# Optimization experiments

Hardware: AMD Instinct MI355X
Metric: run time of the kernel (lower is better)

## Reference

```python
import jax, jax.numpy as jnp
import numpy as np

WALL, SRC_REAL, SRC_IMAG, DELAY_REAL, DELAY_IMAG = 0, 1, 2, 3, 4
DELAY_STEP = 8
MAX_PHASE_NORM = 2.0
READOUT_THRESHOLD = 0.35
PHASE_CLASSES = 8


def conv2d(x, w, b, pad):
    y = jax.lax.conv_general_dilated(x, w, (1, 1), [(pad, pad), (pad, pad)],
                                     dimension_numbers=('NCHW', 'OIHW', 'NCHW'))
    return y + b[None, :, None, None]


def clamp_phase(r, i):
    mag = jnp.sqrt(r * r + i * i + 1e-8)
    s = jnp.minimum(MAX_PHASE_NORM / mag, 1.0)
    return r * s, i * s


def neighbor_sum(x):
    # zero-padded 4-neighbor shift-and-sum stencil
    p = jnp.pad(x, ((0, 0), (0, 0), (1, 1), (1, 1)))
    return (p[:, :, 2:, 1:-1] + p[:, :, :-2, 1:-1] +
            p[:, :, 1:-1, 2:] + p[:, :, 1:-1, :-2])


def setup_inputs() -> dict:
    key = jax.random.key(0)
    ks = jax.random.split(key, 8)
    B, H, W, WD = 8, 256, 256, 32
    CIN = 6 + 4  # INPUT_CHANNELS + 4 (state_r, state_i, frontier_r, frontier_i)
    x = jax.random.normal(ks[0], (B, 6, H, W), jnp.float32)
    target = jax.random.randint(ks[1], (B, 2), 0, H)
    w_in = jax.random.normal(ks[2], (WD, CIN, 1, 1), jnp.float32) * (1.0 / np.sqrt(CIN))
    b_in = jnp.zeros((WD,), jnp.float32)
    w_up = jax.random.normal(ks[3], (WD, WD + CIN, 3, 3), jnp.float32) * (1.0 / np.sqrt((WD + CIN) * 9))
    b_up = jnp.zeros((WD,), jnp.float32)
    w_gate = jax.random.normal(ks[4], (1, WD + CIN, 1, 1), jnp.float32) * (1.0 / np.sqrt(WD + CIN))
    b_gate = jnp.zeros((1,), jnp.float32)
    angle = jnp.float32(0.0)
    decay_logit = jnp.float32(3.9)
    return dict(x=x, target=target, w_in=w_in, b_in=b_in, w_up=w_up, b_up=b_up,
                w_gate=w_gate, b_gate=b_gate, angle=angle, decay_logit=decay_logit, steps=16)


def reference(x, target, w_in, b_in, w_up, b_up, w_gate, b_gate, angle, decay_logit, steps):
    wall = x[:, WALL:WALL + 1]
    free = 1.0 - wall
    state_r = x[:, SRC_REAL:SRC_REAL + 1] * free
    state_i = x[:, SRC_IMAG:SRC_IMAG + 1] * free
    frontier_r, frontier_i = state_r, state_i
    h = jnp.tanh(conv2d(jnp.concatenate([x, state_r, state_i, frontier_r, frontier_i], 1), w_in, b_in, 0)) * free

    ang = jnp.tanh(angle) * 0.02
    cos_a, sin_a = jnp.cos(ang), jnp.sin(ang)
    decay = 0.95 + 0.05 * jax.nn.sigmoid(decay_logit)
    delay_r = x[:, DELAY_REAL:DELAY_REAL + 1]
    delay_i = x[:, DELAY_IMAG:DELAY_IMAG + 1]

    def body(carry, step):
        s_r, s_i, f_r, f_i, hh = carry
        inc_r = neighbor_sum(f_r)
        inc_i = neighbor_sum(f_i)
        is_delay = (step == DELAY_STEP).astype(x.dtype)
        inc_r = inc_r + is_delay * delay_r
        inc_i = inc_i + is_delay * delay_i
        source = jnp.concatenate([hh, x, s_r, s_i, f_r, f_i], 1)
        g = 0.998 + 0.002 * jax.nn.sigmoid(conv2d(source, w_gate, b_gate, 0))
        inc_r = inc_r * g
        inc_i = inc_i * g
        rot_r = inc_r * cos_a - inc_i * sin_a
        rot_i = inc_r * sin_a + inc_i * cos_a
        inc_r, inc_i = rot_r * free, rot_i * free
        inc_r, inc_i = clamp_phase(inc_r, inc_i)
        pre_wall = ((jnp.abs(inc_r) + jnp.abs(inc_i)) * wall).mean()
        s_r, s_i = clamp_phase(decay * s_r + inc_r, decay * s_i + inc_i)
        s_r = s_r * free
        s_i = s_i * free
        hh = jnp.tanh(0.8 * hh + conv2d(source, w_up, b_up, 1)) * free
        st = jnp.concatenate([s_r, s_i], 1)
        return (s_r, s_i, inc_r, inc_i, hh), (st, pre_wall)

    carry0 = (state_r, state_i, frontier_r, frontier_i, h)
    _, (sts, pre_walls) = jax.lax.scan(body, carry0, jnp.arange(1, steps + 1))
    state0 = jnp.concatenate([state_r, state_i], 1)
    states = jnp.concatenate([state0[None], sts], 0)  # [steps+1, B, 2, H, W]
    final = states[-1]

    diffs = states[1:] - states[:-1]
    delta = jnp.mean(jnp.sqrt(jnp.mean(diffs ** 2, axis=(1, 2, 3, 4))))
    norm_by_step = jnp.mean(jnp.sqrt(jnp.sum(states ** 2, axis=2)))
    sat = (jnp.abs(final) > 4.0).astype(jnp.float32).mean()
    pw = pre_walls.mean()
    norm = jnp.sqrt(jnp.sum(final ** 2, axis=1, keepdims=True))
    leak = ((norm > 0.5) & (wall > 0.5)).astype(jnp.float32).mean()
    stats = jnp.stack([delta, norm_by_step, sat, pw, leak])

    b = jnp.arange(final.shape[0])
    vec = final[b, :, target[:, 0], target[:, 1]]  # [B, 2]
    k = jnp.arange(PHASE_CLASSES)
    theta = 2.0 * jnp.pi * k / PHASE_CLASSES
    phases = jnp.stack([jnp.cos(theta), jnp.sin(theta)], axis=1)  # [K, 2]
    mag = jnp.sqrt(jnp.sum(vec ** 2, axis=1) + 1e-8)
    none = (READOUT_THRESHOLD - mag) * 12.0
    phase_logits = (vec @ phases.T - READOUT_THRESHOLD) * 12.0
    logits = jnp.concatenate([none[:, None], phase_logits], axis=1)
    return logits, stats
```

## Files before the change

### kernel.cpp

```cpp
#include <hip/hip_runtime.h>
#include <hip/hip_bf16.h>

#define HW2D 65536
#define NPIX 524288
#define NB 8
#define PW 258
#define PP 66564
#define NSTEPS 16
#define RHH 2064
#define RTT 4128
#define ROWB 8256

typedef __hip_bfloat16 bf16;
typedef unsigned long long u64;
typedef __attribute__((ext_vector_type(8))) short short8;
typedef __attribute__((ext_vector_type(4))) float f32x4;

__device__ __forceinline__ unsigned short f2bfu(float v){
  bf16 h = __float2bfloat16(v); return *(unsigned short*)&h;
}
__device__ __forceinline__ float blo(unsigned int w){ return __uint_as_float(w<<16); }
__device__ __forceinline__ float bhi(unsigned int w){ return __uint_as_float(w & 0xffff0000u); }
__device__ __forceinline__ float tanh_a(float z){
  return z*__builtin_amdgcn_rsqf(fmaf(z, z, 1.0f));
}
__device__ __forceinline__ float fast_sigmoid(float z){
  return 1.0f/(1.0f + __expf(-z));
}
__device__ __forceinline__ unsigned char f2fp8(float v){
  return (unsigned char)(__builtin_amdgcn_cvt_pk_fp8_f32(v, 0.f, 0, false) & 0xFF);
}
__device__ __forceinline__ int chmap(int m){ return (m>>1) + (m&1)*16; }

__global__ void k_setup(const float* __restrict__ w_up, const float* __restrict__ w_gate,
                        const float* angle, const float* decay_logit,
                        u64* __restrict__ WB8, short8* __restrict__ WB16,
                        float* ST, float* PRM){
  int t = threadIdx.x;
  for (int i = t; i < 64*32; i += 256) ST[i] = 0.0f;
  if (t == 0){
    float ang = tanhf(angle[0])*0.02f;
    PRM[0] = cosf(ang);
    PRM[1] = sinf(ang);
    PRM[2] = 0.95f + 0.05f/(1.0f+expf(-decay_logit[0]));
  }
  int lane = t & 63;
  int r_ = lane & 15, g = lane >> 4;
  for (int slot = t>>6; slot < 19; slot += 4){
    u64 v = 0;
    #pragma unroll
    for (int j=0;j<8;j++){
      float w = 0.f;
      int ch = chmap(g*8+j);
      if (slot < 18){
        int tile = slot/9, s = slot%9;
        int oc = tile*16 + r_;
        int dy=s/3, dx=s%3;
        w = w_up[((oc*42+ch)*3+dy)*3+dx];
        if (s==4 && oc==ch) w += 0.8f;
      } else {
        if (r_==0) w = w_gate[ch];
      }
      v |= ((u64)f2fp8(w)) << (8*j);
    }
    WB8[slot*64+lane] = v;
  }
  for (int slot = t>>6; slot < 11; slot += 4){
    short8 v;
    #pragma unroll
    for (int j=0;j<8;j++){
      float w = 0.f;
      int tt = (g&1)*8 + j;
      int tapsel = g>>1;
      if (slot < 10){
        int tile = slot/5, s2 = slot%5;
        int tap = 2*s2 + tapsel;
        int oc = tile*16 + r_;
        if (tap <= 8 && tt < 10){
          int src = (tt<4) ? (38+tt) : (32+(tt-4));
          int dy=tap/3, dx=tap%3;
          w = w_up[((oc*42+src)*3+dy)*3+dx];
        }
      } else {
        if (r_==0 && tapsel==0 && tt<10){
          int src = (tt<4) ? (38+tt) : (32+(tt-4));
          w = w_gate[src];
        }
      }
      v[j] = (short)f2bfu(w);
    }
    WB16[slot*64+lane] = v;
  }
}

__global__ void k_init(const float* __restrict__ x, const float* __restrict__ w_in,
                       const float* __restrict__ b_in,
                       float* __restrict__ WALL,
                       unsigned char* __restrict__ HH0, unsigned char* __restrict__ HH1,
                       unsigned char* __restrict__ TAIL0, unsigned char* __restrict__ TAIL1,
                       float* ST){
  int tid = threadIdx.x;
  int i = blockIdx.x*256 + tid;
  float v = 0.0f;
  if (i < NB*PP){
    int b = i / PP, pp_ = i % PP;
    int row = pp_ / PW, col = pp_ % PW;
    size_t rb = (size_t)(b*PW + row);
    if (row == 0 || row == 257 || col == 0 || col == 257){
      #pragma unroll
      for (int g=0; g<4; g++){
        size_t a = (rb*4+g)*RHH + (size_t)col*8;
        *(uint2*)(HH0+a) = (uint2){0,0};
        *(uint2*)(HH1+a) = (uint2){0,0};
      }
      #pragma unroll
      for (int h=0; h<2; h++){
        size_t a = (rb*2+h)*RTT + (size_t)col*16;
        *(uint4*)(TAIL0+a) = (uint4){0,0,0,0};
        *(uint4*)(TAIL1+a) = (uint4){0,0,0,0};
      }
    } else {
      int y = row-1, xc = col-1;
      int rem = (y<<8) + xc;
      const float* xb = x + (size_t)b*6*HW2D;
      float wall = xb[rem];
      float fre = 1.0f - wall;
      float s_r = xb[HW2D + rem]*fre;
      float s_i = xb[2*HW2D + rem]*fre;
      WALL[b*HW2D + rem] = wall;
      float src10[10];
      src10[0]=wall;
      #pragma unroll
      for (int c=1;c<6;c++) src10[c]=xb[c*HW2D+rem];
      src10[6]=s_r; src10[7]=s_i; src10[8]=s_r; src10[9]=s_i;
      float hv[32];
      #pragma unroll
      for (int c=0;c<32;c++){
        float a = b_in[c];
        #pragma unroll
        for (int k=0;k<10;k++) a += w_in[c*10+k]*src10[k];
        hv[c] = tanh_a(a)*fre;
      }
      unsigned int words[8];
      #pragma unroll
      for (int w=0;w<8;w++){
        int lo = __builtin_amdgcn_cvt_pk_fp8_f32(hv[2*w], hv[16+2*w], 0, false);
        words[w] = (unsigned int)__builtin_amdgcn_cvt_pk_fp8_f32(hv[2*w+1], hv[17+2*w], lo, true);
      }
      #pragma unroll
      for (int g=0; g<4; g++){
        *(uint2*)(HH0 + (rb*4+g)*RHH + (size_t)col*8) = (uint2){words[2*g], words[2*g+1]};
      }
      unsigned short tv[16];
      tv[0]=f2bfu(s_r); tv[1]=f2bfu(s_i); tv[2]=f2bfu(s_r); tv[3]=f2bfu(s_i);
      #pragma unroll
      for (int c=0;c<6;c++) tv[4+c] = f2bfu(src10[c]);
      #pragma unroll
      for (int c=10;c<16;c++) tv[c] = 0;
      #pragma unroll
      for (int h=0; h<2; h++){
        short8 vv;
        #pragma unroll
        for (int j=0;j<8;j++) vv[j] = (short)tv[h*8+j];
        *(short8*)(TAIL0 + (rb*2+h)*RTT + (size_t)col*16) = vv;
        *(short8*)(TAIL1 + (rb*2+h)*RTT + (size_t)col*16) = vv;
      }
      v = __builtin_amdgcn_sqrtf(s_r*s_r + s_i*s_i);
    }
  }
  #pragma unroll
  for (int off=32; off>0; off>>=1) v += __shfl_down(v, off);
  if ((tid&63)==0 && v != 0.0f)
    atomicAdd(&ST[(blockIdx.x & 63)*32 + 16], v);
}

__global__ __launch_bounds__(256) void k_step(
    const unsigned char* __restrict__ HHo, unsigned char* __restrict__ HHn,
    const unsigned char* __restrict__ TAILo, unsigned char* __restrict__ TAILn,
    const float* __restrict__ WALL,
    const u64* __restrict__ WB8, const short8* __restrict__ WB16,
    const float* __restrict__ b_up, const float* __restrict__ x,
    const float* __restrict__ b_gate, const float* __restrict__ PRM,
    float* ST, int step){
  int bid = blockIdx.x;
  int b = bid & 7, y = bid >> 3;
  int tid = threadIdx.x;
  int wv = tid >> 6, lane = tid & 63;
  int r_ = lane & 15, g = lane >> 4;
  int px0 = wv*64 + r_;

  const unsigned char* Tc = TAILo + (size_t)(b*PW + y + 1)*ROWB + (size_t)(tid+1)*16;
  unsigned int sw  = *(const unsigned int*)(Tc);
  unsigned int fu  = *(const unsigned int*)(Tc - ROWB + 4);
  unsigned int fd  = *(const unsigned int*)(Tc + ROWB + 4);
  unsigned int fl  = *(const unsigned int*)(Tc - 16 + 4);
  unsigned int fr2 = *(const unsigned int*)(Tc + 16 + 4);
  float dlr = 0.f, dli = 0.f;
  if (step==8){
    const float* xb = x + (size_t)b*6*HW2D;
    int rem = (y<<8)+tid;
    dlr = xb[3*HW2D+rem]; dli = xb[4*HW2D+rem];
  }
  float wallB = WALL[b*HW2D + (y<<8) + tid];
  float ca = PRM[0], sa = PRM[1], dec = PRM[2];

  const unsigned char* Hrow = HHo + (size_t)(b*PW + y)*ROWB + (size_t)g*RHH + (size_t)px0*8;
  const unsigned char* Trow = TAILo + (size_t)(b*PW + y)*ROWB + (size_t)(g&1)*RTT + (size_t)px0*16;
  const unsigned char* Tzero = TAILo + (size_t)(b*PW)*ROWB + (size_t)(g&1)*RTT + (size_t)px0*16;
  int gb = g >> 1;
  const unsigned char* tb0 = Trow + (size_t)((0+gb)/3)*ROWB + (size_t)((0+gb)%3)*16;
  const unsigned char* tb1 = Trow + (size_t)((2+gb)/3)*ROWB + (size_t)((2+gb)%3)*16;
  const unsigned char* tb2 = Trow + (size_t)((4+gb)/3)*ROWB + (size_t)((4+gb)%3)*16;
  const unsigned char* tb3 = Trow + (size_t)((6+gb)/3)*ROWB + (size_t)((6+gb)%3)*16;
  const unsigned char* tb4 = gb ? Tzero : (Trow + 2*ROWB + 2*16);
  const u64* wb8l = WB8 + lane;
  const short8* wb16l = WB16 + lane;

  f32x4 acc[4][2], accg[4];
  #pragma unroll
  for (int mt=0;mt<4;mt++){
    acc[mt][0] = (f32x4){0.f,0.f,0.f,0.f};
    acc[mt][1] = (f32x4){0.f,0.f,0.f,0.f};
    accg[mt]   = (f32x4){0.f,0.f,0.f,0.f};
  }

  __builtin_amdgcn_s_setprio(1);
  #pragma unroll
  for (int s=0;s<9;s++){
    u64 b0 = wb8l[s*64], b1 = wb8l[(9+s)*64];
    u64 aH[4];
    #pragma unroll
    for (int mt=0;mt<4;mt++)
      aH[mt] = *(const u64*)(Hrow + (size_t)((s/3)*ROWB) + ((s%3)*8 + mt*128));
    #pragma unroll
    for (int mt=0;mt<4;mt++){
      acc[mt][0] = __builtin_amdgcn_mfma_f32_16x16x32_fp8_fp8((long)b0, (long)aH[mt], acc[mt][0], 0,0,0);
      acc[mt][1] = __builtin_amdgcn_mfma_f32_16x16x32_fp8_fp8((long)b1, (long)aH[mt], acc[mt][1], 0,0,0);
    }
    if (s==4){
      u64 bg = wb8l[18*64];
      #pragma unroll
      for (int mt=0;mt<4;mt++)
        accg[mt] = __builtin_amdgcn_mfma_f32_16x16x32_fp8_fp8((long)bg, (long)aH[mt], accg[mt], 0,0,0);
    }
  }
  #pragma unroll
  for (int s2=0;s2<5;s2++){
    short8 b0 = wb16l[s2*64], b1 = wb16l[(5+s2)*64];
    const unsigned char* tb = (s2==0)?tb0:(s2==1)?tb1:(s2==2)?tb2:(s2==3)?tb3:tb4;
    short8 aT[4];
    #pragma unroll
    for (int mt=0;mt<4;mt++)
      aT[mt] = *(const short8*)(tb + mt*256);
    #pragma unroll
    for (int mt=0;mt<4;mt++){
      acc[mt][0] = __builtin_amdgcn_mfma_f32_16x16x32_bf16(b0, aT[mt], acc[mt][0], 0,0,0);
      acc[mt][1] = __builtin_amdgcn_mfma_f32_16x16x32_bf16(b1, aT[mt], acc[mt][1], 0,0,0);
    }
    if (s2==2){
      short8 bgt = wb16l[10*64];
      #pragma unroll
      for (int mt=0;mt<4;mt++)
        accg[mt] = __builtin_amdgcn_mfma_f32_16x16x32_bf16(bgt, aT[mt], accg[mt], 0,0,0);
    }
  }
  __builtin_amdgcn_s_setprio(0);

  float ga0 = __shfl(accg[0][0], r_);
  float ga1 = __shfl(accg[1][0], r_);
  float ga2 = __shfl(accg[2][0], r_);
  float ga3 = __shfl(accg[3][0], r_);
  float gpre = (g==0) ? ga0 : (g==1) ? ga1 : (g==2) ? ga2 : ga3;

  const float* wallrow = WALL + (size_t)b*HW2D + (y<<8);
  const float4* bup4 = (const float4*)b_up;
  float4 bb0 = bup4[g];
  float4 bb1 = bup4[4+g];
  unsigned char* Hn = HHn + ((size_t)(b*PW + y + 1)*4 + g)*RHH;
  #pragma unroll
  for (int mt=0;mt<4;mt++){
    int px = px0 + mt*16;
    float fre = 1.0f - wallrow[px];
    float tA0 = tanh_a(acc[mt][0][0] + bb0.x)*fre;
    float tB0 = tanh_a(acc[mt][1][0] + bb1.x)*fre;
    float tA1 = tanh_a(acc[mt][0][1] + bb0.y)*fre;
    float tB1 = tanh_a(acc[mt][1][1] + bb1.y)*fre;
    float tA2 = tanh_a(acc[mt][0][2] + bb0.z)*fre;
    float tB2 = tanh_a(acc[mt][1][2] + bb1.z)*fre;
    float tA3 = tanh_a(acc[mt][0][3] + bb0.w)*fre;
    float tB3 = tanh_a(acc[mt][1][3] + bb1.w)*fre;
    int w0 = __builtin_amdgcn_cvt_pk_fp8_f32(tA0, tB0, 0, false);
    w0 = __builtin_amdgcn_cvt_pk_fp8_f32(tA1, tB1, w0, true);
    int w1 = __builtin_amdgcn_cvt_pk_fp8_f32(tA2, tB2, 0, false);
    w1 = __builtin_amdgcn_cvt_pk_fp8_f32(tA3, tB3, w1, true);
    *(uint2*)(Hn + (size_t)(px+1)*8) = (uint2){(unsigned)w0, (unsigned)w1};
  }

  float s_r = blo(sw), s_i = bhi(sw);
  float incr = blo(fu) + blo(fd) + blo(fl) + blo(fr2) + dlr;
  float inci = bhi(fu) + bhi(fd) + bhi(fl) + bhi(fr2) + dli;
  float fre = 1.0f - wallB;
  float a = gpre + b_gate[0];
  float gg = 0.998f + 0.002f*fast_sigmoid(a);
  incr *= gg; inci *= gg;
  float rr = incr*ca - inci*sa;
  float ri = incr*sa + inci*ca;
  incr = rr*fre; inci = ri*fre;
  float m1 = fmaf(incr,incr, fmaf(inci,inci, 1e-8f));
  float sc2 = fminf(2.0f*__builtin_amdgcn_rsqf(m1), 1.0f);
  incr *= sc2; inci *= sc2;
  float pw = (fabsf(incr)+fabsf(inci))*wallB;
  float nr = dec*s_r + incr, ni = dec*s_i + inci;
  float m2 = fmaf(nr,nr, fmaf(ni,ni, 1e-8f));
  sc2 = fminf(2.0f*__builtin_amdgcn_rsqf(m2), 1.0f);
  nr = nr*sc2*fre; ni = ni*sc2*fre;
  ushort4 pk;
  pk.x = f2bfu(nr); pk.y = f2bfu(ni); pk.z = f2bfu(incr); pk.w = f2bfu(inci);
  *(ushort4*)(TAILn + (size_t)(b*PW + y + 1)*ROWB + (size_t)(tid+1)*16) = pk;
  float d2 = (nr-s_r)*(nr-s_r)+(ni-s_i)*(ni-s_i);
  float nrm = __builtin_amdgcn_sqrtf(nr*nr+ni*ni);
  #pragma unroll
  for (int off=32; off>0; off>>=1){
    d2  += __shfl_down(d2, off);
    nrm += __shfl_down(nrm, off);
    pw  += __shfl_down(pw, off);
  }
  if (step==16){
    float sat = (fabsf(nr)>4.0f ? 1.0f:0.0f) + (fabsf(ni)>4.0f ? 1.0f:0.0f);
    float nn = __builtin_amdgcn_sqrtf(nr*nr+ni*ni);
    float leak = (nn>0.5f && wallB>0.5f) ? 1.0f : 0.0f;
    #pragma unroll
    for (int off=32; off>0; off>>=1){
      sat  += __shfl_down(sat, off);
      leak += __shfl_down(leak, off);
    }
    if (lane==0){
      float* st = ST + ((bid*4+wv) & 63)*32;
      atomicAdd(&st[18], sat);
      atomicAdd(&st[19], leak);
    }
  }
  if (lane==0){
    float* st = ST + ((bid*4+wv) & 63)*32;
    atomicAdd(&st[step-1], d2);
    atomicAdd(&st[16],     nrm);
    atomicAdd(&st[17],     pw);
  }
}

__global__ void k_final(const unsigned char* __restrict__ TAIL, const int* __restrict__ target,
                        const float* __restrict__ ST, float* __restrict__ out){
  int t = threadIdx.x;
  if (t < 8){
    int ty = target[2*t], tx = target[2*t+1];
    unsigned int sw = *(const unsigned int*)(TAIL + (size_t)(t*PW+ty+1)*ROWB + (size_t)(tx+1)*16);
    float vr = blo(sw), vi = bhi(sw);
    float mag = sqrtf(vr*vr+vi*vi+1e-8f);
    out[t*9] = (0.35f - mag)*12.0f;
    #pragma unroll
    for (int k=0;k<8;k++){
      float th = 6.283185307179586f * (float)k / 8.0f;
      out[t*9+1+k] = (vr*cosf(th)+vi*sinf(th) - 0.35f)*12.0f;
    }
  }
  float tot[20];
  #pragma unroll
  for (int i=0;i<20;i++){
    float v = ST[t*32 + i];
    #pragma unroll
    for (int off=32; off>0; off>>=1) v += __shfl_down(v, off);
    tot[i] = v;
  }
  if (t == 0){
    float d = 0.0f;
    #pragma unroll
    for (int s=0;s<16;s++) d += sqrtf(tot[s]/1048576.0f);
    out[72] = d/16.0f;
    out[73] = tot[16]/8912896.0f;
    out[74] = tot[18]/1048576.0f;
    out[75] = tot[17]/(524288.0f*16.0f);
    out[76] = tot[19]/524288.0f;
  }
}

extern "C" void kernel_launch(void* const* d_in, const int* in_sizes, int n_in,
                              void* d_out, int out_size, void* d_ws, size_t ws_size,
                              hipStream_t stream) {
  const float* x       = (const float*)d_in[0];
  const int*   target  = (const int*)  d_in[1];
  const float* w_in    = (const float*)d_in[2];
  const float* b_in    = (const float*)d_in[3];
  const float* w_up    = (const float*)d_in[4];
  const float* b_up    = (const float*)d_in[5];
  const float* w_gate  = (const float*)d_in[6];
  const float* b_gate  = (const float*)d_in[7];
  const float* angle   = (const float*)d_in[8];
  const float* decay_l = (const float*)d_in[9];
  float* out = (float*)d_out;

  char* ws = (char*)d_ws;
  size_t off = 0;
  unsigned char* HH0 = (unsigned char*)(ws+off); off += (size_t)NB*PP*32;
  unsigned char* HH1 = (unsigned char*)(ws+off); off += (size_t)NB*PP*32;
  unsigned char* TAIL0=(unsigned char*)(ws+off); off += (size_t)NB*PP*32;
  unsigned char* TAIL1=(unsigned char*)(ws+off); off += (size_t)NB*PP*32;
  float* WALL = (float*)(ws+off); off += (size_t)NPIX*4;
  u64* WB8 = (u64*)(ws+off); off += (size_t)19*64*8;
  short8* WB16 = (short8*)(ws+off); off += (size_t)11*64*16;
  float* ST = (float*)(ws+off); off += (size_t)64*32*4;
  float* PRM = (float*)(ws+off); off += 16*4;

  k_setup<<<1,256,0,stream>>>(w_up, w_gate, angle, decay_l, WB8, WB16, ST, PRM);
  k_init<<<(NB*PP+255)/256,256,0,stream>>>(x, w_in, b_in, WALL, HH0, HH1,
                                           TAIL0, TAIL1, ST);

  unsigned char *hho=HH0, *hhn=HH1, *tlo=TAIL0, *tln=TAIL1;
  for (int t=1;t<=NSTEPS;t++){
    k_step<<<2048,256,0,stream>>>(hho, hhn, tlo, tln, WALL,
                                  WB8, WB16, b_up, x, b_gate, PRM, ST, t);
    unsigned char* tc=hho; hho=hhn; hhn=tc;
    tc=tlo; tlo=tln; tln=tc;
  }
  k_final<<<1,64,0,stream>>>(tlo, target, ST, out);
}
```

Baseline: 504.3 us.

## Split step kernel across 8 waves, passing gate through shared memory

Doubles the block size of the step kernel to 512 threads so each wave computes 32 pixels (2 MFMA tiles) instead of 64. This cuts per-thread accumulator registers and raises the number of waves available to hide memory latency. Because wave and pixel indices no longer line up, the gate pre-activation is passed through LDS behind a block barrier, and only the first 256 threads run the stencil and state update. In exchange it adds a barrier, leaves half the threads idle in the elementwise tail, and loads weights redundantly in more waves.

Result: slower. 580.5 us (+15.1%).

```diff
diff --git a/kernel.cpp b/kernel.cpp
--- a/kernel.cpp
+++ b/kernel.cpp
@@ -174,7 +174,7 @@
     atomicAdd(&ST[(blockIdx.x & 63)*32 + 16], v);
 }
 
-__global__ __launch_bounds__(256) void k_step(
+__global__ __launch_bounds__(512) void k_step(
     const unsigned char* __restrict__ HHo, unsigned char* __restrict__ HHn,
     const unsigned char* __restrict__ TAILo, unsigned char* __restrict__ TAILn,
     const float* __restrict__ WALL,
@@ -182,27 +182,13 @@
     const float* __restrict__ b_up, const float* __restrict__ x,
     const float* __restrict__ b_gate, const float* __restrict__ PRM,
     float* ST, int step){
+  __shared__ float lgate[256];
   int bid = blockIdx.x;
   int b = bid & 7, y = bid >> 3;
   int tid = threadIdx.x;
   int wv = tid >> 6, lane = tid & 63;
   int r_ = lane & 15, g = lane >> 4;
-  int px0 = wv*64 + r_;
-
-  const unsigned char* Tc = TAILo + (size_t)(b*PW + y + 1)*ROWB + (size_t)(tid+1)*16;
-  unsigned int sw  = *(const unsigned int*)(Tc);
-  unsigned int fu  = *(const unsigned int*)(Tc - ROWB + 4);
-  unsigned int fd  = *(const unsigned int*)(Tc + ROWB + 4);
-  unsigned int fl  = *(const unsigned int*)(Tc - 16 + 4);
-  unsigned int fr2 = *(const unsigned int*)(Tc + 16 + 4);
-  float dlr = 0.f, dli = 0.f;
-  if (step==8){
-    const float* xb = x + (size_t)b*6*HW2D;
-    int rem = (y<<8)+tid;
-    dlr = xb[3*HW2D+rem]; dli = xb[4*HW2D+rem];
-  }
-  float wallB = WALL[b*HW2D + (y<<8) + tid];
-  float ca = PRM[0], sa = PRM[1], dec = PRM[2];
+  int px0 = wv*32 + r_;
 
   const unsigned char* Hrow = HHo + (size_t)(b*PW + y)*ROWB + (size_t)g*RHH + (size_t)px0*8;
   const unsigned char* Trow = TAILo + (size_t)(b*PW + y)*ROWB + (size_t)(g&1)*RTT + (size_t)px0*16;
@@ -216,135 +202,152 @@
   const u64* wb8l = WB8 + lane;
   const short8* wb16l = WB16 + lane;
 
-  f32x4 acc[4][2], accg[4];
-  #pragma unroll
-  for (int mt=0;mt<4;mt++){
-    acc[mt][0] = (f32x4){0.f,0.f,0.f,0.f};
-    acc[mt][1] = (f32x4){0.f,0.f,0.f,0.f};
-    accg[mt]   = (f32x4){0.f,0.f,0.f,0.f};
-  }
+  f32x4 a00=(f32x4){0.f,0.f,0.f,0.f}, a01=(f32x4){0.f,0.f,0.f,0.f};
+  f32x4 a10=(f32x4){0.f,0.f,0.f,0.f}, a11=(f32x4){0.f,0.f,0.f,0.f};
+  f32x4 ag0=(f32x4){0.f,0.f,0.f,0.f}, ag1=(f32x4){0.f,0.f,0.f,0.f};
 
   __builtin_amdgcn_s_setprio(1);
   #pragma unroll
   for (int s=0;s<9;s++){
     u64 b0 = wb8l[s*64], b1 = wb8l[(9+s)*64];
-    u64 aH[4];
-    #pragma unroll
-    for (int mt=0;mt<4;mt++)
-      aH[mt] = *(const u64*)(Hrow + (size_t)((s/3)*ROWB) + ((s%3)*8 + mt*128));
-    #pragma unroll
-    for (int mt=0;mt<4;mt++){
-      acc[mt][0] = __builtin_amdgcn_mfma_f32_16x16x32_fp8_fp8((long)b0, (long)aH[mt], acc[mt][0], 0,0,0);
-      acc[mt][1] = __builtin_amdgcn_mfma_f32_16x16x32_fp8_fp8((long)b1, (long)aH[mt], acc[mt][1], 0,0,0);
-    }
+    const int aoff = (s/3)*ROWB + (s%3)*8;
+    u64 hA = *(const u64*)(Hrow + aoff);
+    u64 hB = *(const u64*)(Hrow + aoff + 128);
+    a00 = __builtin_amdgcn_mfma_f32_16x16x32_fp8_fp8((long)b0, (long)hA, a00, 0,0,0);
+    a01 = __builtin_amdgcn_mfma_f32_16x16x32_fp8_fp8((long)b1, (long)hA, a01, 0,0,0);
+    a10 = __builtin_amdgcn_mfma_f32_16x16x32_fp8_fp8((long)b0, (long)hB, a10, 0,0,0);
+    a11 = __builtin_amdgcn_mfma_f32_16x16x32_fp8_fp8((long)b1, (long)hB, a11, 0,0,0);
     if (s==4){
       u64 bg = wb8l[18*64];
-      #pragma unroll
-      for (int mt=0;mt<4;mt++)
-        accg[mt] = __builtin_amdgcn_mfma_f32_16x16x32_fp8_fp8((long)bg, (long)aH[mt], accg[mt], 0,0,0);
+      ag0 = __builtin_amdgcn_mfma_f32_16x16x32_fp8_fp8((long)bg, (long)hA, ag0, 0,0,0);
+      ag1 = __builtin_amdgcn_mfma_f32_16x16x32_fp8_fp8((long)bg, (long)hB, ag1, 0,0,0);
     }
   }
   #pragma unroll
   for (int s2=0;s2<5;s2++){
     short8 b0 = wb16l[s2*64], b1 = wb16l[(5+s2)*64];
     const unsigned char* tb = (s2==0)?tb0:(s2==1)?tb1:(s2==2)?tb2:(s2==3)?tb3:tb4;
-    short8 aT[4];
-    #pragma unroll
-    for (int mt=0;mt<4;mt++)
-      aT[mt] = *(const short8*)(tb + mt*256);
-    #pragma unroll
-    for (int mt=0;mt<4;mt++){
-      acc[mt][0] = __builtin_amdgcn_mfma_f32_16x16x32_bf16(b0, aT[mt], acc[mt][0], 0,0,0);
-      acc[mt][1] = __builtin_amdgcn_mfma_f32_16x16x32_bf16(b1, aT[mt], acc[mt][1], 0,0,0);
-    }
+    short8 tA = *(const short8*)(tb);
+    short8 tB = *(const short8*)(tb + 256);
+    a00 = __builtin_amdgcn_mfma_f32_16x16x32_bf16(b0, tA, a00, 0,0,0);
+    a01 = __builtin_amdgcn_mfma_f32_16x16x32_bf16(b1, tA, a01, 0,0,0);
+    a10 = __builtin_amdgcn_mfma_f32_16x16x32_bf16(b0, tB, a10, 0,0,0);
+    a11 = __builtin_amdgcn_mfma_f32_16x16x32_bf16(b1, tB, a11, 0,0,0);
     if (s2==2){
       short8 bgt = wb16l[10*64];
-      #pragma unroll
-      for (int mt=0;mt<4;mt++)
-        accg[mt] = __builtin_amdgcn_mfma_f32_16x16x32_bf16(bgt, aT[mt], accg[mt], 0,0,0);
+      ag0 = __builtin_amdgcn_mfma_f32_16x16x32_bf16(bgt, tA, ag0, 0,0,0);
+      ag1 = __builtin_amdgcn_mfma_f32_16x16x32_bf16(bgt, tB, ag1, 0,0,0);
     }
   }
   __builtin_amdgcn_s_setprio(0);
 
-  float ga0 = __shfl(accg[0][0], r_);
-  float ga1 = __shfl(accg[1][0], r_);
-  float ga2 = __shfl(accg[2][0], r_);
-  float ga3 = __shfl(accg[3][0], r_);
-  float gpre = (g==0) ? ga0 : (g==1) ? ga1 : (g==2) ? ga2 : ga3;
-
-  const float* wallrow = WALL + (size_t)b*HW2D + (y<<8);
-  const float4* bup4 = (const float4*)b_up;
-  float4 bb0 = bup4[g];
-  float4 bb1 = bup4[4+g];
-  unsigned char* Hn = HHn + ((size_t)(b*PW + y + 1)*4 + g)*RHH;
-  #pragma unroll
-  for (int mt=0;mt<4;mt++){
-    int px = px0 + mt*16;
-    float fre = 1.0f - wallrow[px];
-    float tA0 = tanh_a(acc[mt][0][0] + bb0.x)*fre;
-    float tB0 = tanh_a(acc[mt][1][0] + bb1.x)*fre;
-    float tA1 = tanh_a(acc[mt][0][1] + bb0.y)*fre;
-    float tB1 = tanh_a(acc[mt][1][1] + bb1.y)*fre;
-    float tA2 = tanh_a(acc[mt][0][2] + bb0.z)*fre;
-    float tB2 = tanh_a(acc[mt][1][2] + bb1.z)*fre;
-    float tA3 = tanh_a(acc[mt][0][3] + bb0.w)*fre;
-    float tB3 = tanh_a(acc[mt][1][3] + bb1.w)*fre;
-    int w0 = __builtin_amdgcn_cvt_pk_fp8_f32(tA0, tB0, 0, false);
-    w0 = __builtin_amdgcn_cvt_pk_fp8_f32(tA1, tB1, w0, true);
-    int w1 = __builtin_amdgcn_cvt_pk_fp8_f32(tA2, tB2, 0, false);
-    w1 = __builtin_amdgcn_cvt_pk_fp8_f32(tA3, tB3, w1, true);
-    *(uint2*)(Hn + (size_t)(px+1)*8) = (uint2){(unsigned)w0, (unsigned)w1};
-  }
-
-  float s_r = blo(sw), s_i = bhi(sw);
-  float incr = blo(fu) + blo(fd) + blo(fl) + blo(fr2) + dlr;
-  float inci = bhi(fu) + bhi(fd) + bhi(fl) + bhi(fr2) + dli;
-  float fre = 1.0f - wallB;
-  float a = gpre + b_gate[0];
-  float gg = 0.998f + 0.002f*fast_sigmoid(a);
-  incr *= gg; inci *= gg;
-  float rr = incr*ca - inci*sa;
-  float ri = incr*sa + inci*ca;
-  incr = rr*fre; inci = ri*fre;
-  float m1 = fmaf(incr,incr, fmaf(inci,inci, 1e-8f));
-  float sc2 = fminf(2.0f*__builtin_amdgcn_rsqf(m1), 1.0f);
-  incr *= sc2; inci *= sc2;
-  float pw = (fabsf(incr)+fabsf(inci))*wallB;
-  float nr = dec*s_r + incr, ni = dec*s_i + inci;
-  float m2 = fmaf(nr,nr, fmaf(ni,ni, 1e-8f));
-  sc2 = fminf(2.0f*__builtin_amdgcn_rsqf(m2), 1.0f);
-  nr = nr*sc2*fre; ni = ni*sc2*fre;
-  ushort4 pk;
-  pk.x = f2bfu(nr); pk.y = f2bfu(ni); pk.z = f2bfu(incr); pk.w = f2bfu(inci);
-  *(ushort4*)(TAILn + (size_t)(b*PW + y + 1)*ROWB + (size_t)(tid+1)*16) = pk;
-  float d2 = (nr-s_r)*(nr-s_r)+(ni-s_i)*(ni-s_i);
-  float nrm = __builtin_amdgcn_sqrtf(nr*nr+ni*ni);
-  #pragma unroll
-  for (int off=32; off>0; off>>=1){
-    d2  += __shfl_down(d2, off);
-    nrm += __shfl_down(nrm, off);
-    pw  += __shfl_down(pw, off);
-  }
-  if (step==16){
-    float sat = (fabsf(nr)>4.0f ? 1.0f:0.0f) + (fabsf(ni)>4.0f ? 1.0f:0.0f);
-    float nn = __builtin_amdgcn_sqrtf(nr*nr+ni*ni);
-    float leak = (nn>0.5f && wallB>0.5f) ? 1.0f : 0.0f;
+  if (lane < 16){
+    lgate[wv*32 + lane]      = ag0[0];
+    lgate[wv*32 + 16 + lane] = ag1[0];
+  }
+
+  unsigned int sw=0, fu=0, fd=0, fl=0, fr2=0;
+  float wallB = 0.f, dlr = 0.f, dli = 0.f;
+  if (tid < 256){
+    const unsigned char* Tc = TAILo + (size_t)(b*PW + y + 1)*ROWB + (size_t)(tid+1)*16;
+    sw  = *(const unsigned int*)(Tc);
+    fu  = *(const unsigned int*)(Tc - ROWB + 4);
+    fd  = *(const unsigned int*)(Tc + ROWB + 4);
+    fl  = *(const unsigned int*)(Tc - 16 + 4);
+    fr2 = *(const unsigned int*)(Tc + 16 + 4);
+    wallB = WALL[b*HW2D + (y<<8) + tid];
+    if (step==8){
+      const float* xb = x + (size_t)b*6*HW2D;
+      int rem = (y<<8)+tid;
+      dlr = xb[3*HW2D+rem]; dli = xb[4*HW2D+rem];
+    }
+  }
+
+  {
+    const float* wallrow = WALL + (size_t)b*HW2D + (y<<8);
+    const float4* bup4 = (const float4*)b_up;
+    float4 bb0 = bup4[g];
+    float4 bb1 = bup4[4+g];
+    unsigned char* Hn = HHn + ((size_t)(b*PW + y + 1)*4 + g)*RHH;
+    #pragma unroll
+    for (int mt=0;mt<2;mt++){
+      f32x4 A = mt ? a10 : a00;
+      f32x4 B = mt ? a11 : a01;
+      int px = px0 + mt*16;
+      float fre = 1.0f - wallrow[px];
+      float tA0 = tanh_a(A[0] + bb0.x)*fre;
+      float tB0 = tanh_a(B[0] + bb1.x)*fre;
+      float tA1 = tanh_a(A[1] + bb0.y)*fre;
+      float tB1 = tanh_a(B[1] + bb1.y)*fre;
+      float tA2 = tanh_a(A[2] + bb0.z)*fre;
+      float tB2 = tanh_a(B[2] + bb1.z)*fre;
+      float tA3 = tanh_a(A[3] + bb0.w)*fre;
+      float tB3 = tanh_a(B[3] + bb1.w)*fre;
+      int w0 = __builtin_amdgcn_cvt_pk_fp8_f32(tA0, tB0, 0, false);
+      w0 = __builtin_amdgcn_cvt_pk_fp8_f32(tA1, tB1, w0, true);
+      int w1 = __builtin_amdgcn_cvt_pk_fp8_f32(tA2, tB2, 0, false);
+      w1 = __builtin_amdgcn_cvt_pk_fp8_f32(tA3, tB3, w1, true);
+      *(uint2*)(Hn + (size_t)(px+1)*8) = (uint2){(unsigned)w0, (unsigned)w1};
+    }
+  }
+
+  __builtin_amdgcn_sched_barrier(0);
+  asm volatile("s_waitcnt lgkmcnt(0)" ::: "memory");
+  __builtin_amdgcn_s_barrier();
+  __builtin_amdgcn_sched_barrier(0);
+
+  if (tid < 256){
+    float ca = PRM[0], sa = PRM[1], dec = PRM[2];
+    float s_r = blo(sw), s_i = bhi(sw);
+    float incr = blo(fu) + blo(fd) + blo(fl) + blo(fr2) + dlr;
+    float inci = bhi(fu) + bhi(fd) + bhi(fl) + bhi(fr2) + dli;
+    float fre = 1.0f - wallB;
+    float a = lgate[tid] + b_gate[0];
+    float gg = 0.998f + 0.002f*fast_sigmoid(a);
+    incr *= gg; inci *= gg;
+    float rr = incr*ca - inci*sa;
+    float ri = incr*sa + inci*ca;
+    incr = rr*fre; inci = ri*fre;
+    float m1 = fmaf(incr,incr, fmaf(inci,inci, 1e-8f));
+    float sc2 = fminf(2.0f*__builtin_amdgcn_rsqf(m1), 1.0f);
+    incr *= sc2; inci *= sc2;
+    float pw = (fabsf(incr)+fabsf(inci))*wallB;
+    float nr = dec*s_r + incr, ni = dec*s_i + inci;
+    float m2 = fmaf(nr,nr, fmaf(ni,ni, 1e-8f));
+    sc2 = fminf(2.0f*__builtin_amdgcn_rsqf(m2), 1.0f);
+    nr = nr*sc2*fre; ni = ni*sc2*fre;
+    ushort4 pk;
+    pk.x = f2bfu(nr); pk.y = f2bfu(ni); pk.z = f2bfu(incr); pk.w = f2bfu(inci);
+    *(ushort4*)(TAILn + (size_t)(b*PW + y + 1)*ROWB + (size_t)(tid+1)*16) = pk;
+    float d2 = (nr-s_r)*(nr-s_r)+(ni-s_i)*(ni-s_i);
+    float nrm = __builtin_amdgcn_sqrtf(nr*nr+ni*ni);
     #pragma unroll
     for (int off=32; off>0; off>>=1){
-      sat  += __shfl_down(sat, off);
-      leak += __shfl_down(leak, off);
+      d2  += __shfl_down(d2, off);
+      nrm += __shfl_down(nrm, off);
+      pw  += __shfl_down(pw, off);
+    }
+    if (step==16){
+      float sat = (fabsf(nr)>4.0f ? 1.0f:0.0f) + (fabsf(ni)>4.0f ? 1.0f:0.0f);
+      float nn = __builtin_amdgcn_sqrtf(nr*nr+ni*ni);
+      float leak = (nn>0.5f && wallB>0.5f) ? 1.0f : 0.0f;
+      #pragma unroll
+      for (int off=32; off>0; off>>=1){
+        sat  += __shfl_down(sat, off);
+        leak += __shfl_down(leak, off);
+      }
+      if (lane==0){
+        float* st = ST + ((bid*4+wv) & 63)*32;
+        atomicAdd(&st[18], sat);
+        atomicAdd(&st[19], leak);
+      }
     }
     if (lane==0){
       float* st = ST + ((bid*4+wv) & 63)*32;
-      atomicAdd(&st[18], sat);
-      atomicAdd(&st[19], leak);
-    }
-  }
-  if (lane==0){
-    float* st = ST + ((bid*4+wv) & 63)*32;
-    atomicAdd(&st[step-1], d2);
-    atomicAdd(&st[16],     nrm);
-    atomicAdd(&st[17],     pw);
+      atomicAdd(&st[step-1], d2);
+      atomicAdd(&st[16],     nrm);
+      atomicAdd(&st[17],     pw);
+    }
   }
 }
 
@@ -416,7 +419,7 @@
 
   unsigned char *hho=HH0, *hhn=HH1, *tlo=TAIL0, *tln=TAIL1;
   for (int t=1;t<=NSTEPS;t++){
-    k_step<<<2048,256,0,stream>>>(hho, hhn, tlo, tln, WALL,
+    k_step<<<2048,512,0,stream>>>(hho, hhn, tlo, tln, WALL,
                                   WB8, WB16, b_up, x, b_gate, PRM, ST, t);
     unsigned char* tc=hho; hho=hhn; hhn=tc;
     tc=tlo; tlo=tln; tln=tc;
```
